# Optimization experiments

Measured on AMD Instinct MI355X. Metric: run time of the kernel, lower is better.

## Reference

```python
import jax, jax.numpy as jnp
import numpy as np

N = 100000       # nodes
E = 1600000      # edges (avg degree 16)
F_NODE = 32
F_GLOB = 16
H = 64           # hidden_channels
OUT = 64         # output_dim
N_LAYERS = 3


def setup_inputs() -> dict:
    key = jax.random.key(0)
    ks = jax.random.split(key, 16)
    s = 0.05
    inp = {
        "x": jax.random.normal(ks[0], (N, F_NODE), jnp.float32),
        "edge_index": jax.random.randint(ks[1], (2, E), 0, N, jnp.int64)
                      if jax.config.jax_enable_x64 else
                      jax.random.randint(ks[1], (2, E), 0, N, jnp.int32).astype(jnp.int32),
        "global_features": jax.random.normal(ks[2], (F_GLOB,), jnp.float32),
        "w_node": jax.random.normal(ks[3], (F_NODE, H), jnp.float32) * s,
        "b_node": jnp.zeros((H,), jnp.float32),
        "w_glob": jax.random.normal(ks[4], (F_GLOB, H), jnp.float32) * s,
        "b_glob": jnp.zeros((H,), jnp.float32),
        "w_c0": jax.random.normal(ks[5], (H, H), jnp.float32) * s,
        "b_c0": jnp.zeros((H,), jnp.float32),
        "w_c1": jax.random.normal(ks[6], (H, H), jnp.float32) * s,
        "b_c1": jnp.zeros((H,), jnp.float32),
        "w_c2": jax.random.normal(ks[7], (H, H), jnp.float32) * s,
        "b_c2": jnp.zeros((H,), jnp.float32),
        "w_fc1": jax.random.normal(ks[8], (2 * H, H), jnp.float32) * s,
        "b_fc1": jnp.zeros((H,), jnp.float32),
        "w_fc2": jax.random.normal(ks[9], (H, OUT), jnp.float32) * s,
        "b_fc2": jnp.zeros((OUT,), jnp.float32),
    }
    return inp


def _gcn_conv(x, src, dst, norm, w, b):
    # PyG GCNConv: h = x @ W; out[dst] += norm * h[src]; out += bias
    h = x @ w                                  # [N, H]
    msg = h[src] * norm[:, None]               # [E', H] gather
    out = jax.ops.segment_sum(msg, dst, num_segments=N)  # scatter-add
    return out + b


def reference(x, edge_index, global_features,
              w_node, b_node, w_glob, b_glob,
              w_c0, b_c0, w_c1, b_c1, w_c2, b_c2,
              w_fc1, b_fc1, w_fc2, b_fc2):
    # add self-loops (GCNConv default)
    loop = jnp.arange(N, dtype=edge_index.dtype)
    src = jnp.concatenate([edge_index[0], loop])
    dst = jnp.concatenate([edge_index[1], loop])
    # symmetric normalization deg^{-1/2} (edge weights = 1, deg from targets)
    deg = jax.ops.segment_sum(jnp.ones_like(dst, dtype=x.dtype), dst, num_segments=N)
    dis = jax.lax.rsqrt(deg)                   # deg >= 1 via self-loops
    norm = dis[src] * dis[dst]                 # [E']

    h = x @ w_node + b_node                    # node embedding
    for w, b in ((w_c0, b_c0), (w_c1, b_c1), (w_c2, b_c2)):
        h = jax.nn.relu(_gcn_conv(h, src, dst, norm, w, b))
        # dropout is identity in eval mode

    x_graph = jnp.mean(h, axis=0)                       # [H]
    x_global = jax.nn.relu(global_features @ w_glob + b_glob)  # [H]
    xc = jnp.concatenate([x_graph, x_global], axis=0)   # [2H]
    out = jax.nn.relu(xc @ w_fc1 + b_fc1) @ w_fc2 + b_fc2
    return out
```

## Files before the change

### kernel.cpp

```cpp
#include <hip/hip_runtime.h>

#define N_NODES 100000
#define N_EDGES 1600000
#define F_NODE  32
#define F_GLOB  16
#define HDIM    64
#define OUTDIM  64
#define PBLK    512
#define CHUNK   3125
#define EPT     13
#define NSH     128
#define SHN     782
#define SCAP    13568
#define NTILE   (N_NODES / 16)

typedef unsigned short u16;
typedef unsigned int   u32;
typedef __attribute__((ext_vector_type(8))) short short8v;
typedef __attribute__((ext_vector_type(4))) float f32x4;

__device__ __forceinline__ u16 f2b(float f) {
    u32 u = __float_as_uint(f);
    return (u16)((u + 0x7fffu + ((u >> 16) & 1u)) >> 16);
}
__device__ __forceinline__ float blo(u32 p) { return __uint_as_float(p << 16); }
__device__ __forceinline__ float bhi(u32 p) { return __uint_as_float(p & 0xffff0000u); }


__global__ void __launch_bounds__(256)
k_part(const int* __restrict__ src, const int* __restrict__ dst,
       int* __restrict__ shcnt, int2* __restrict__ stage) {
    __shared__ int lcnt[NSH];
    __shared__ int gbase[NSH];
    int t = threadIdx.x;
    for (int i = t; i < NSH; i += 256) lcnt[i] = 0;
    __syncthreads();
    int e0 = blockIdx.x * CHUNK;
    int n = N_EDGES - e0; if (n > CHUNK) n = CHUNK; if (n < 0) n = 0;
    int2 ev[EPT]; int rk[EPT]; int sh[EPT];
    #pragma unroll
    for (int j = 0; j < EPT; ++j) {
        int i = t + j * 256;
        if (i < n) {
            int sv = __builtin_nontemporal_load(&src[e0 + i]);
            int dv = __builtin_nontemporal_load(&dst[e0 + i]);
            int k = dv / SHN;
            ev[j] = make_int2(sv, dv);
            sh[j] = k;
            rk[j] = atomicAdd(&lcnt[k], 1);
        }
    }
    __syncthreads();
    for (int i = t; i < NSH; i += 256)
        gbase[i] = atomicAdd(&shcnt[i], lcnt[i]);
    __syncthreads();
    #pragma unroll
    for (int j = 0; j < EPT; ++j) {
        int i = t + j * 256;
        if (i < n) {
            int p = gbase[sh[j]] + rk[j];
            if (p < SCAP) stage[(size_t)sh[j] * SCAP + p] = ev[j];
        }
    }
}

__global__ void __launch_bounds__(1024)
k_build(const int2* __restrict__ stage, const int* __restrict__ shcnt,
        int* __restrict__ rowptr, float* __restrict__ dis, int* __restrict__ col) {
    __shared__ int shc[NSH];
    __shared__ int hist[1024];
    __shared__ int A[1024];
    __shared__ int B[1024];
    int t = threadIdx.x;
    int s = blockIdx.x;
    if (t < NSH) shc[t] = shcnt[t];
    hist[t] = 0;
    __syncthreads();
    int sb = 0;
    for (int q = 0; q < s; ++q) sb += shc[q];
    int n = shc[s]; if (n > SCAP) n = SCAP;
    const int2* st = stage + (size_t)s * SCAP;
    int v0 = s * SHN;
    for (int p = t; p < n; p += 1024)
        atomicAdd(&hist[st[p].y - v0], 1);
    __syncthreads();
    A[t] = hist[t];
    __syncthreads();
    int* cur = A; int* nxt = B;
    for (int ofs = 1; ofs < 1024; ofs <<= 1) {
        nxt[t] = cur[t] + (t >= ofs ? cur[t - ofs] : 0);
        __syncthreads();
        int* tmp = cur; cur = nxt; nxt = tmp;
    }
    int v = v0 + t;
    if (t < SHN && v < N_NODES) {
        rowptr[v] = sb + cur[t] - hist[t];
        dis[v] = rsqrtf((float)(hist[t] + 1));
    }
    if (s == NSH - 1 && t == 0) rowptr[N_NODES] = N_EDGES;
    nxt[t] = sb + cur[t] - hist[t];
    __syncthreads();
    for (int p = t; p < n; p += 1024) {
        int2 ed = st[p];
        int slot = atomicAdd(&nxt[ed.y - v0], 1);
        col[slot] = ed.x;
    }
}


__global__ void __launch_bounds__(256)
k_cvt(const float* __restrict__ x, u16* __restrict__ xb) {
    int i = blockIdx.x * 256 + threadIdx.x;
    if ((size_t)i * 8 >= (size_t)N_NODES * F_NODE) return;
    float4 a = ((const float4*)x)[i * 2];
    float4 b = ((const float4*)x)[i * 2 + 1];
    uint4 o;
    o.x = (u32)f2b(a.x) | ((u32)f2b(a.y) << 16);
    o.y = (u32)f2b(a.z) | ((u32)f2b(a.w) << 16);
    o.z = (u32)f2b(b.x) | ((u32)f2b(b.y) << 16);
    o.w = (u32)f2b(b.z) | ((u32)f2b(b.w) << 16);
    ((uint4*)xb)[i] = o;
}


template<int K, bool BIAS, bool DIS>
__global__ void __launch_bounds__(256)
k_mfma(const u16* __restrict__ Amat, const float* __restrict__ W,
       const float* __restrict__ bias, const float* __restrict__ dis,
       u16* __restrict__ out) {
    int t = threadIdx.x, wid = t >> 6, l = t & 63;
    int tile = blockIdx.x * 4 + wid;
    if (tile >= NTILE) return;
    int lr = l & 15, kc = l >> 4;
    constexpr int KB = K / 32;
    short8v bfrag[4][KB];
    #pragma unroll
    for (int ct = 0; ct < 4; ++ct)
        #pragma unroll
        for (int kb = 0; kb < KB; ++kb)
            #pragma unroll
            for (int j = 0; j < 8; ++j)
                bfrag[ct][kb][j] = (short)f2b(W[(kb * 32 + kc * 8 + j) * HDIM + ct * 16 + lr]);
    int r0 = tile * 16;
    const u16* arow = Amat + (size_t)(r0 + lr) * K + kc * 8;
    short8v a[KB];
    #pragma unroll
    for (int kb = 0; kb < KB; ++kb)
        a[kb] = *(const short8v*)(arow + kb * 32);
    f32x4 acc[4];
    #pragma unroll
    for (int ct = 0; ct < 4; ++ct) acc[ct] = (f32x4){0.f, 0.f, 0.f, 0.f};
    #pragma unroll
    for (int ct = 0; ct < 4; ++ct)
        #pragma unroll
        for (int kb = 0; kb < KB; ++kb)
            acc[ct] = __builtin_amdgcn_mfma_f32_16x16x32_bf16(a[kb], bfrag[ct][kb], acc[ct], 0, 0, 0);
    float dv[4];
    #pragma unroll
    for (int j = 0; j < 4; ++j)
        dv[j] = DIS ? dis[r0 + kc * 4 + j] : 1.f;
    #pragma unroll
    for (int ct = 0; ct < 4; ++ct) {
        float bb = BIAS ? bias[ct * 16 + lr] : 0.f;
        #pragma unroll
        for (int j = 0; j < 4; ++j) {
            int row = r0 + kc * 4 + j;
            float val = acc[ct][j];
            if (BIAS) val += bb;
            if (DIS)  val *= dv[j];
            out[(size_t)row * HDIM + ct * 16 + lr] = f2b(val);
        }
    }
}


__global__ void __launch_bounds__(256)
k_pull(const u16* __restrict__ hw, const int* __restrict__ rowptr,
       const int* __restrict__ col, const float* __restrict__ dis,
       const float* __restrict__ b, u16* __restrict__ hout) {
    int t = threadIdx.x, wid = t >> 6, lane = t & 63;
    int g = lane >> 3, sub = lane & 7;
    int v = blockIdx.x * 32 + wid * 8 + g;
    const u16* hws = hw + sub * 8;
    uint4 sv = *(const uint4*)(hws + (size_t)v * HDIM);
    float acc[8];
    acc[0] = blo(sv.x); acc[1] = bhi(sv.x);
    acc[2] = blo(sv.y); acc[3] = bhi(sv.y);
    acc[4] = blo(sv.z); acc[5] = bhi(sv.z);
    acc[6] = blo(sv.w); acc[7] = bhi(sv.w);
    int s0 = rowptr[v], s1 = rowptr[v + 1];
    int i = s0;
    for (; i + 2 <= s1; i += 2) {
        int c0 = col[i], c1 = col[i + 1];
        uint4 a0 = *(const uint4*)(hws + (size_t)c0 * HDIM);
        uint4 a1 = *(const uint4*)(hws + (size_t)c1 * HDIM);
        acc[0] += blo(a0.x); acc[1] += bhi(a0.x);
        acc[2] += blo(a0.y); acc[3] += bhi(a0.y);
        acc[4] += blo(a0.z); acc[5] += bhi(a0.z);
        acc[6] += blo(a0.w); acc[7] += bhi(a0.w);
        acc[0] += blo(a1.x); acc[1] += bhi(a1.x);
        acc[2] += blo(a1.y); acc[3] += bhi(a1.y);
        acc[4] += blo(a1.z); acc[5] += bhi(a1.z);
        acc[6] += blo(a1.w); acc[7] += bhi(a1.w);
    }
    if (i < s1) {
        int c0 = col[i];
        uint4 a0 = *(const uint4*)(hws + (size_t)c0 * HDIM);
        acc[0] += blo(a0.x); acc[1] += bhi(a0.x);
        acc[2] += blo(a0.y); acc[3] += bhi(a0.y);
        acc[4] += blo(a0.z); acc[5] += bhi(a0.z);
        acc[6] += blo(a0.w); acc[7] += bhi(a0.w);
    }
    float4 b0 = *(const float4*)&b[sub * 8];
    float4 b1 = *(const float4*)&b[sub * 8 + 4];
    float bb[8] = {b0.x, b0.y, b0.z, b0.w, b1.x, b1.y, b1.z, b1.w};
    float dv = dis[v];
    u32 r[8];
    #pragma unroll
    for (int k = 0; k < 8; ++k) {
        float val = fmaxf(bb[k] + dv * acc[k], 0.f);
        u32 u = __float_as_uint(val);
        r[k] = (u + 0x7fffu + ((u >> 16) & 1u)) >> 16;
    }
    uint4 pk;
    pk.x = r[0] | (r[1] << 16); pk.y = r[2] | (r[3] << 16);
    pk.z = r[4] | (r[5] << 16); pk.w = r[6] | (r[7] << 16);
    *(uint4*)(hout + (size_t)v * HDIM + sub * 8) = pk;
}


__global__ void k_mean(const u16* __restrict__ h, float* __restrict__ partial) {
    __shared__ float lds[256];
    int t = threadIdx.x;
    int f = t & 63, g = t >> 6;
    float acc = 0.f;
    for (int v = blockIdx.x * 4 + g; v < N_NODES; v += gridDim.x * 4)
        acc += __uint_as_float((u32)h[(size_t)v * HDIM + f] << 16);
    lds[t] = acc;
    __syncthreads();
    if (t < 64)
        partial[blockIdx.x * 64 + t] = lds[t] + lds[t + 64] + lds[t + 128] + lds[t + 192];
}

__global__ void __launch_bounds__(256)
k_final(const float* __restrict__ partial,
        const float* __restrict__ gfeat,
        const float* __restrict__ wg, const float* __restrict__ bg,
        const float* __restrict__ w1, const float* __restrict__ b1,
        const float* __restrict__ w2, const float* __restrict__ b2,
        float* __restrict__ out) {
    __shared__ float red[4][HDIM];
    __shared__ float xc[2 * HDIM];
    __shared__ float hid[HDIM];
    int t = threadIdx.x, g = t >> 6, lane = t & 63;
    float s = 0.f;
    for (int p = g * 64; p < (g + 1) * 64; ++p) s += partial[p * 64 + lane];
    red[g][lane] = s;
    __syncthreads();
    if (g == 0) {
        xc[lane] = (red[0][lane] + red[1][lane] + red[2][lane] + red[3][lane])
                   / (float)N_NODES;
    } else if (g == 1) {
        float gacc = bg[lane];
        for (int k = 0; k < F_GLOB; ++k) gacc += gfeat[k] * wg[k * HDIM + lane];
        xc[HDIM + lane] = fmaxf(gacc, 0.f);
    }
    __syncthreads();
    float hacc = 0.f;
    for (int k = g * 32; k < (g + 1) * 32; ++k) hacc += xc[k] * w1[k * HDIM + lane];
    red[g][lane] = hacc;
    __syncthreads();
    if (g == 0)
        hid[lane] = fmaxf(b1[lane] + red[0][lane] + red[1][lane]
                          + red[2][lane] + red[3][lane], 0.f);
    __syncthreads();
    float oacc = 0.f;
    for (int k = g * 16; k < (g + 1) * 16; ++k) oacc += hid[k] * w2[k * OUTDIM + lane];
    red[g][lane] = oacc;
    __syncthreads();
    if (g == 0)
        out[lane] = b2[lane] + red[0][lane] + red[1][lane]
                  + red[2][lane] + red[3][lane];
}


extern "C" void kernel_launch(void* const* d_in, const int* in_sizes, int n_in,
                              void* d_out, int out_size, void* d_ws, size_t ws_size,
                              hipStream_t stream) {
    const float* x      = (const float*)d_in[0];
    const int*   eidx   = (const int*)d_in[1];
    const float* gfeat  = (const float*)d_in[2];
    const float* w_node = (const float*)d_in[3];
    const float* b_node = (const float*)d_in[4];
    const float* w_glob = (const float*)d_in[5];
    const float* b_glob = (const float*)d_in[6];
    const float* w_c[3] = {(const float*)d_in[7], (const float*)d_in[9], (const float*)d_in[11]};
    const float* b_c[3] = {(const float*)d_in[8], (const float*)d_in[10], (const float*)d_in[12]};
    const float* w_fc1  = (const float*)d_in[13];
    const float* b_fc1  = (const float*)d_in[14];
    const float* w_fc2  = (const float*)d_in[15];
    const float* b_fc2  = (const float*)d_in[16];
    float* out = (float*)d_out;

    const int* srcp = eidx;
    const int* dstp = eidx + N_EDGES;

    char* ws = (char*)d_ws;
    size_t off = 0;
    auto alloc = [&](size_t bytes) -> void* {
        void* p = ws + off;
        off = (off + bytes + 255) & ~(size_t)255;
        return p;
    };
    int*   rowptr  = (int*)  alloc((size_t)(N_NODES + 1) * 4);
    int*   shcnt   = (int*)  alloc(NSH * 4);
    float* dis     = (float*)alloc((size_t)N_NODES * 4);
    int*   col     = (int*)  alloc((size_t)N_EDGES * 4);
    int2*  stage   = (int2*) alloc((size_t)NSH * SCAP * 8);
    u16*   xb      = (u16*)  alloc((size_t)N_NODES * F_NODE * 2);
    u16*   hbuf    = (u16*)  alloc((size_t)N_NODES * HDIM * 2);
    u16*   hwbuf   = (u16*)  alloc((size_t)N_NODES * HDIM * 2);
    float* partial = (float*)alloc(256 * 64 * 4);

    hipMemsetAsync(shcnt, 0, NSH * 4, stream);

    k_part <<<PBLK, 256, 0, stream>>>(srcp, dstp, shcnt, stage);
    k_build<<<NSH, 1024, 0, stream>>>(stage, shcnt, rowptr, dis, col);

    int mb = (NTILE + 3) / 4;
    int cb = ((N_NODES * F_NODE / 8) + 255) / 256;

    k_cvt<<<cb, 256, 0, stream>>>(x, xb);
    k_mfma<32, true, false><<<mb, 256, 0, stream>>>(xb, w_node, b_node, nullptr, hbuf);
    k_mfma<64, false, true><<<mb, 256, 0, stream>>>(hbuf, w_c[0], nullptr, dis, hwbuf);
    k_pull<<<3125, 256, 0, stream>>>(hwbuf, rowptr, col, dis, b_c[0], hbuf);
    for (int l = 1; l < 3; ++l) {
        k_mfma<64, false, true><<<mb, 256, 0, stream>>>(hbuf, w_c[l], nullptr, dis, hwbuf);
        k_pull<<<3125, 256, 0, stream>>>(hwbuf, rowptr, col, dis, b_c[l], hbuf);
    }
    k_mean <<<256, 256, 0, stream>>>(hbuf, partial);
    k_final<<<1, 256, 0, stream>>>(partial, gfeat, w_glob, b_glob,
                                   w_fc1, b_fc1, w_fc2, b_fc2, out);
}
```

Before: 324.2 us.

## Degree-sort pull nodes, fuse f32 convert and mean, persistent MFMA grid

Adds a degree histogram in k_build plus a scan and permutation kernel, so the pull kernels process nodes grouped by in-degree and wavefront divergence in the neighbour loop drops. Removes the separate fp32-to-bf16 conversion kernel by converting x inside the first MFMA kernel. Fuses the mean reduction into the last pull kernel with shuffles and per-block partials. MFMA kernels become a persistent grid of 512 blocks, and the pull loop is unrolled by four. The cost is two extra small kernels and a less regular memory access order in the pull kernels, where each wave's output rows are now scattered.

```diff
diff --git a/kernel.cpp b/kernel.cpp
--- a/kernel.cpp
+++ b/kernel.cpp
@@ -13,6 +13,8 @@
 #define SHN     782
 #define SCAP    13568
 #define NTILE   (N_NODES / 16)
+#define MFB     512
+#define NPB     3125
 
 typedef unsigned short u16;
 typedef unsigned int   u32;
@@ -66,15 +68,18 @@
 
 __global__ void __launch_bounds__(1024)
 k_build(const int2* __restrict__ stage, const int* __restrict__ shcnt,
-        int* __restrict__ rowptr, float* __restrict__ dis, int* __restrict__ col) {
+        int* __restrict__ rowptr, float* __restrict__ dis, int* __restrict__ col,
+        int* __restrict__ deg, int* __restrict__ gbins) {
     __shared__ int shc[NSH];
     __shared__ int hist[1024];
     __shared__ int A[1024];
     __shared__ int B[1024];
+    __shared__ int dbin[64];
     int t = threadIdx.x;
     int s = blockIdx.x;
     if (t < NSH) shc[t] = shcnt[t];
     hist[t] = 0;
+    if (t < 64) dbin[t] = 0;
     __syncthreads();
     int sb = 0;
     for (int q = 0; q < s; ++q) sb += shc[q];
@@ -93,13 +98,17 @@
         int* tmp = cur; cur = nxt; nxt = tmp;
     }
     int v = v0 + t;
-    if (t < SHN && v < N_NODES) {
+    bool valid = (t < SHN && v < N_NODES);
+    if (valid) {
         rowptr[v] = sb + cur[t] - hist[t];
         dis[v] = rsqrtf((float)(hist[t] + 1));
+        deg[v] = hist[t];
+        atomicAdd(&dbin[hist[t] < 63 ? hist[t] : 63], 1);
     }
     if (s == NSH - 1 && t == 0) rowptr[N_NODES] = N_EDGES;
     nxt[t] = sb + cur[t] - hist[t];
     __syncthreads();
+    if (t < 64 && dbin[t]) atomicAdd(&gbins[t], dbin[t]);
     for (int p = t; p < n; p += 1024) {
         int2 ed = st[p];
         int slot = atomicAdd(&nxt[ed.y - v0], 1);
@@ -107,32 +116,49 @@
     }
 }
 
-
-__global__ void __launch_bounds__(256)
-k_cvt(const float* __restrict__ x, u16* __restrict__ xb) {
-    int i = blockIdx.x * 256 + threadIdx.x;
-    if ((size_t)i * 8 >= (size_t)N_NODES * F_NODE) return;
-    float4 a = ((const float4*)x)[i * 2];
-    float4 b = ((const float4*)x)[i * 2 + 1];
-    uint4 o;
-    o.x = (u32)f2b(a.x) | ((u32)f2b(a.y) << 16);
-    o.y = (u32)f2b(a.z) | ((u32)f2b(a.w) << 16);
-    o.z = (u32)f2b(b.x) | ((u32)f2b(b.y) << 16);
-    o.w = (u32)f2b(b.z) | ((u32)f2b(b.w) << 16);
-    ((uint4*)xb)[i] = o;
-}
-
-
-template<int K, bool BIAS, bool DIS>
-__global__ void __launch_bounds__(256)
-k_mfma(const u16* __restrict__ Amat, const float* __restrict__ W,
+__global__ void k_dscan(const int* __restrict__ gbins, int* __restrict__ cursor) {
+    __shared__ int a[64];
+    int t = threadIdx.x;
+    a[t] = gbins[t];
+    __syncthreads();
+    if (t == 0) { int run = 0; for (int i = 0; i < 64; ++i) { int c = a[i]; a[i] = run; run += c; } }
+    __syncthreads();
+    cursor[t] = a[t];
+}
+
+__global__ void __launch_bounds__(256)
+k_dperm(const int* __restrict__ deg, int* __restrict__ cursor, int* __restrict__ perm) {
+    __shared__ int lb[64];
+    __shared__ int base[64];
+    int t = threadIdx.x;
+    if (t < 64) lb[t] = 0;
+    __syncthreads();
+    int bin[4], rk[4];
+    #pragma unroll
+    for (int j = 0; j < 4; ++j) {
+        int v = blockIdx.x * 1024 + j * 256 + t;
+        if (v < N_NODES) {
+            int d = deg[v]; bin[j] = d < 63 ? d : 63;
+            rk[j] = atomicAdd(&lb[bin[j]], 1);
+        } else bin[j] = -1;
+    }
+    __syncthreads();
+    if (t < 64) base[t] = atomicAdd(&cursor[t], lb[t]);
+    __syncthreads();
+    #pragma unroll
+    for (int j = 0; j < 4; ++j)
+        if (bin[j] >= 0) perm[base[bin[j]] + rk[j]] = blockIdx.x * 1024 + j * 256 + t;
+}
+
+
+template<int K, bool BIAS, bool DIS, bool F32A>
+__global__ void __launch_bounds__(256)
+k_mfma(const void* __restrict__ Aptr, const float* __restrict__ W,
        const float* __restrict__ bias, const float* __restrict__ dis,
        u16* __restrict__ out) {
+    constexpr int KB = K / 32;
     int t = threadIdx.x, wid = t >> 6, l = t & 63;
-    int tile = blockIdx.x * 4 + wid;
-    if (tile >= NTILE) return;
     int lr = l & 15, kc = l >> 4;
-    constexpr int KB = K / 32;
     short8v bfrag[4][KB];
     #pragma unroll
     for (int ct = 0; ct < 4; ++ct)
@@ -141,46 +167,68 @@
             #pragma unroll
             for (int j = 0; j < 8; ++j)
                 bfrag[ct][kb][j] = (short)f2b(W[(kb * 32 + kc * 8 + j) * HDIM + ct * 16 + lr]);
-    int r0 = tile * 16;
-    const u16* arow = Amat + (size_t)(r0 + lr) * K + kc * 8;
-    short8v a[KB];
-    #pragma unroll
-    for (int kb = 0; kb < KB; ++kb)
-        a[kb] = *(const short8v*)(arow + kb * 32);
-    f32x4 acc[4];
-    #pragma unroll
-    for (int ct = 0; ct < 4; ++ct) acc[ct] = (f32x4){0.f, 0.f, 0.f, 0.f};
-    #pragma unroll
-    for (int ct = 0; ct < 4; ++ct)
-        #pragma unroll
-        for (int kb = 0; kb < KB; ++kb)
-            acc[ct] = __builtin_amdgcn_mfma_f32_16x16x32_bf16(a[kb], bfrag[ct][kb], acc[ct], 0, 0, 0);
-    float dv[4];
-    #pragma unroll
-    for (int j = 0; j < 4; ++j)
-        dv[j] = DIS ? dis[r0 + kc * 4 + j] : 1.f;
-    #pragma unroll
-    for (int ct = 0; ct < 4; ++ct) {
-        float bb = BIAS ? bias[ct * 16 + lr] : 0.f;
-        #pragma unroll
-        for (int j = 0; j < 4; ++j) {
-            int row = r0 + kc * 4 + j;
-            float val = acc[ct][j];
-            if (BIAS) val += bb;
-            if (DIS)  val *= dv[j];
-            out[(size_t)row * HDIM + ct * 16 + lr] = f2b(val);
+    float bb[4];
+    #pragma unroll
+    for (int ct = 0; ct < 4; ++ct) bb[ct] = BIAS ? bias[ct * 16 + lr] : 0.f;
+    int gw = blockIdx.x * 4 + wid;
+    const int nw = MFB * 4;
+    for (int tile = gw; tile < NTILE; tile += nw) {
+        int r0 = tile * 16;
+        short8v a[KB];
+        if (F32A) {
+            const float* arow = (const float*)Aptr + (size_t)(r0 + lr) * K + kc * 8;
+            #pragma unroll
+            for (int kb = 0; kb < KB; ++kb) {
+                float4 f0 = *(const float4*)(arow + kb * 32);
+                float4 f1 = *(const float4*)(arow + kb * 32 + 4);
+                a[kb][0] = (short)f2b(f0.x); a[kb][1] = (short)f2b(f0.y);
+                a[kb][2] = (short)f2b(f0.z); a[kb][3] = (short)f2b(f0.w);
+                a[kb][4] = (short)f2b(f1.x); a[kb][5] = (short)f2b(f1.y);
+                a[kb][6] = (short)f2b(f1.z); a[kb][7] = (short)f2b(f1.w);
+            }
+        } else {
+            const u16* arow = (const u16*)Aptr + (size_t)(r0 + lr) * K + kc * 8;
+            #pragma unroll
+            for (int kb = 0; kb < KB; ++kb)
+                a[kb] = *(const short8v*)(arow + kb * 32);
         }
-    }
-}
-
-
+        f32x4 acc[4];
+        #pragma unroll
+        for (int ct = 0; ct < 4; ++ct) acc[ct] = (f32x4){0.f, 0.f, 0.f, 0.f};
+        #pragma unroll
+        for (int ct = 0; ct < 4; ++ct)
+            #pragma unroll
+            for (int kb = 0; kb < KB; ++kb)
+                acc[ct] = __builtin_amdgcn_mfma_f32_16x16x32_bf16(a[kb], bfrag[ct][kb], acc[ct], 0, 0, 0);
+        float dv[4];
+        #pragma unroll
+        for (int j = 0; j < 4; ++j)
+            dv[j] = DIS ? dis[r0 + kc * 4 + j] : 1.f;
+        #pragma unroll
+        for (int ct = 0; ct < 4; ++ct)
+            #pragma unroll
+            for (int j = 0; j < 4; ++j) {
+                int row = r0 + kc * 4 + j;
+                float val = acc[ct][j];
+                if (BIAS) val += bb[ct];
+                if (DIS)  val *= dv[j];
+                out[(size_t)row * HDIM + ct * 16 + lr] = f2b(val);
+            }
+    }
+}
+
+
+template<bool MEAN>
 __global__ void __launch_bounds__(256)
 k_pull(const u16* __restrict__ hw, const int* __restrict__ rowptr,
        const int* __restrict__ col, const float* __restrict__ dis,
-       const float* __restrict__ b, u16* __restrict__ hout) {
+       const float* __restrict__ b, const int* __restrict__ perm,
+       u16* __restrict__ hout, float* __restrict__ partial) {
+    __shared__ float ms[64];
     int t = threadIdx.x, wid = t >> 6, lane = t & 63;
     int g = lane >> 3, sub = lane & 7;
-    int v = blockIdx.x * 32 + wid * 8 + g;
+    if (MEAN) { if (t < 64) ms[t] = 0.f; __syncthreads(); }
+    int v = perm[blockIdx.x * 32 + wid * 8 + g];
     const u16* hws = hw + sub * 8;
     uint4 sv = *(const uint4*)(hws + (size_t)v * HDIM);
     float acc[8];
@@ -190,20 +238,22 @@
     acc[6] = blo(sv.w); acc[7] = bhi(sv.w);
     int s0 = rowptr[v], s1 = rowptr[v + 1];
     int i = s0;
-    for (; i + 2 <= s1; i += 2) {
-        int c0 = col[i], c1 = col[i + 1];
+    for (; i + 4 <= s1; i += 4) {
+        int c0 = col[i], c1 = col[i + 1], c2 = col[i + 2], c3 = col[i + 3];
         uint4 a0 = *(const uint4*)(hws + (size_t)c0 * HDIM);
         uint4 a1 = *(const uint4*)(hws + (size_t)c1 * HDIM);
-        acc[0] += blo(a0.x); acc[1] += bhi(a0.x);
-        acc[2] += blo(a0.y); acc[3] += bhi(a0.y);
-        acc[4] += blo(a0.z); acc[5] += bhi(a0.z);
-        acc[6] += blo(a0.w); acc[7] += bhi(a0.w);
-        acc[0] += blo(a1.x); acc[1] += bhi(a1.x);
-        acc[2] += blo(a1.y); acc[3] += bhi(a1.y);
-        acc[4] += blo(a1.z); acc[5] += bhi(a1.z);
-        acc[6] += blo(a1.w); acc[7] += bhi(a1.w);
-    }
-    if (i < s1) {
+        uint4 a2 = *(const uint4*)(hws + (size_t)c2 * HDIM);
+        uint4 a3 = *(const uint4*)(hws + (size_t)c3 * HDIM);
+        acc[0] += blo(a0.x) + blo(a1.x); acc[1] += bhi(a0.x) + bhi(a1.x);
+        acc[2] += blo(a0.y) + blo(a1.y); acc[3] += bhi(a0.y) + bhi(a1.y);
+        acc[4] += blo(a0.z) + blo(a1.z); acc[5] += bhi(a0.z) + bhi(a1.z);
+        acc[6] += blo(a0.w) + blo(a1.w); acc[7] += bhi(a0.w) + bhi(a1.w);
+        acc[0] += blo(a2.x) + blo(a3.x); acc[1] += bhi(a2.x) + bhi(a3.x);
+        acc[2] += blo(a2.y) + blo(a3.y); acc[3] += bhi(a2.y) + bhi(a3.y);
+        acc[4] += blo(a2.z) + blo(a3.z); acc[5] += bhi(a2.z) + bhi(a3.z);
+        acc[6] += blo(a2.w) + blo(a3.w); acc[7] += bhi(a2.w) + bhi(a3.w);
+    }
+    for (; i < s1; ++i) {
         int c0 = col[i];
         uint4 a0 = *(const uint4*)(hws + (size_t)c0 * HDIM);
         acc[0] += blo(a0.x); acc[1] += bhi(a0.x);
@@ -215,32 +265,33 @@
     float4 b1 = *(const float4*)&b[sub * 8 + 4];
     float bb[8] = {b0.x, b0.y, b0.z, b0.w, b1.x, b1.y, b1.z, b1.w};
     float dv = dis[v];
+    float o[8];
     u32 r[8];
     #pragma unroll
     for (int k = 0; k < 8; ++k) {
-        float val = fmaxf(bb[k] + dv * acc[k], 0.f);
-        u32 u = __float_as_uint(val);
+        o[k] = fmaxf(bb[k] + dv * acc[k], 0.f);
+        u32 u = __float_as_uint(o[k]);
         r[k] = (u + 0x7fffu + ((u >> 16) & 1u)) >> 16;
     }
     uint4 pk;
     pk.x = r[0] | (r[1] << 16); pk.y = r[2] | (r[3] << 16);
     pk.z = r[4] | (r[5] << 16); pk.w = r[6] | (r[7] << 16);
     *(uint4*)(hout + (size_t)v * HDIM + sub * 8) = pk;
-}
-
-
-__global__ void k_mean(const u16* __restrict__ h, float* __restrict__ partial) {
-    __shared__ float lds[256];
-    int t = threadIdx.x;
-    int f = t & 63, g = t >> 6;
-    float acc = 0.f;
-    for (int v = blockIdx.x * 4 + g; v < N_NODES; v += gridDim.x * 4)
-        acc += __uint_as_float((u32)h[(size_t)v * HDIM + f] << 16);
-    lds[t] = acc;
-    __syncthreads();
-    if (t < 64)
-        partial[blockIdx.x * 64 + t] = lds[t] + lds[t + 64] + lds[t + 128] + lds[t + 192];
-}
+    if (MEAN) {
+        #pragma unroll
+        for (int k = 0; k < 8; ++k) {
+            o[k] += __shfl_xor(o[k], 8);
+            o[k] += __shfl_xor(o[k], 16);
+            o[k] += __shfl_xor(o[k], 32);
+        }
+        if (g == 0)
+            #pragma unroll
+            for (int k = 0; k < 8; ++k) atomicAdd(&ms[sub * 8 + k], o[k]);
+        __syncthreads();
+        if (t < 64) partial[(size_t)blockIdx.x * 64 + t] = ms[t];
+    }
+}
+
 
 __global__ void __launch_bounds__(256)
 k_final(const float* __restrict__ partial,
@@ -254,7 +305,7 @@
     __shared__ float hid[HDIM];
     int t = threadIdx.x, g = t >> 6, lane = t & 63;
     float s = 0.f;
-    for (int p = g * 64; p < (g + 1) * 64; ++p) s += partial[p * 64 + lane];
+    for (int p = g; p < NPB; p += 4) s += partial[(size_t)p * 64 + lane];
     red[g][lane] = s;
     __syncthreads();
     if (g == 0) {
@@ -314,31 +365,33 @@
     };
     int*   rowptr  = (int*)  alloc((size_t)(N_NODES + 1) * 4);
     int*   shcnt   = (int*)  alloc(NSH * 4);
+    int*   gbins   = (int*)  alloc(64 * 4);
+    int*   cursor  = (int*)  alloc(64 * 4);
     float* dis     = (float*)alloc((size_t)N_NODES * 4);
+    int*   deg     = (int*)  alloc((size_t)N_NODES * 4);
+    int*   perm    = (int*)  alloc((size_t)N_NODES * 4);
     int*   col     = (int*)  alloc((size_t)N_EDGES * 4);
     int2*  stage   = (int2*) alloc((size_t)NSH * SCAP * 8);
-    u16*   xb      = (u16*)  alloc((size_t)N_NODES * F_NODE * 2);
     u16*   hbuf    = (u16*)  alloc((size_t)N_NODES * HDIM * 2);
     u16*   hwbuf   = (u16*)  alloc((size_t)N_NODES * HDIM * 2);
-    float* partial = (float*)alloc(256 * 64 * 4);
+    float* partial = (float*)alloc((size_t)NPB * 64 * 4);
 
     hipMemsetAsync(shcnt, 0, NSH * 4, stream);
+    hipMemsetAsync(gbins, 0, 64 * 4, stream);
 
     k_part <<<PBLK, 256, 0, stream>>>(srcp, dstp, shcnt, stage);
-    k_build<<<NSH, 1024, 0, stream>>>(stage, shcnt, rowptr, dis, col);
-
-    int mb = (NTILE + 3) / 4;
-    int cb = ((N_NODES * F_NODE / 8) + 255) / 256;
-
-    k_cvt<<<cb, 256, 0, stream>>>(x, xb);
-    k_mfma<32, true, false><<<mb, 256, 0, stream>>>(xb, w_node, b_node, nullptr, hbuf);
-    k_mfma<64, false, true><<<mb, 256, 0, stream>>>(hbuf, w_c[0], nullptr, dis, hwbuf);
-    k_pull<<<3125, 256, 0, stream>>>(hwbuf, rowptr, col, dis, b_c[0], hbuf);
-    for (int l = 1; l < 3; ++l) {
-        k_mfma<64, false, true><<<mb, 256, 0, stream>>>(hbuf, w_c[l], nullptr, dis, hwbuf);
-        k_pull<<<3125, 256, 0, stream>>>(hwbuf, rowptr, col, dis, b_c[l], hbuf);
-    }
-    k_mean <<<256, 256, 0, stream>>>(hbuf, partial);
+    k_build<<<NSH, 1024, 0, stream>>>(stage, shcnt, rowptr, dis, col, deg, gbins);
+    k_dscan<<<1, 64, 0, stream>>>(gbins, cursor);
+    k_dperm<<<98, 256, 0, stream>>>(deg, cursor, perm);
+
+    k_mfma<32, true, false, true><<<MFB, 256, 0, stream>>>(x, w_node, b_node, nullptr, hbuf);
+    k_mfma<64, false, true, false><<<MFB, 256, 0, stream>>>(hbuf, w_c[0], nullptr, dis, hwbuf);
+    k_pull<false><<<NPB, 256, 0, stream>>>(hwbuf, rowptr, col, dis, b_c[0], perm, hbuf, nullptr);
+    k_mfma<64, false, true, false><<<MFB, 256, 0, stream>>>(hbuf, w_c[1], nullptr, dis, hwbuf);
+    k_pull<false><<<NPB, 256, 0, stream>>>(hwbuf, rowptr, col, dis, b_c[1], perm, hbuf, nullptr);
+    k_mfma<64, false, true, false><<<MFB, 256, 0, stream>>>(hbuf, w_c[2], nullptr, dis, hwbuf);
+    k_pull<true><<<NPB, 256, 0, stream>>>(hwbuf, rowptr, col, dis, b_c[2], perm, hbuf, partial);
+
     k_final<<<1, 256, 0, stream>>>(partial, gfeat, w_glob, b_glob,
                                    w_fc1, b_fc1, w_fc2, b_fc2, out);
 }
```

Result: slower. 465.7 us (+43.6%).
